# Kernel tuning notes

Hardware: AMD Instinct MI355X
Metric: run time of the kernel (lower is better)

## Reference

```python
import jax, jax.numpy as jnp
import numpy as np

B = 16384       # batch size
P = 2           # fixed pooling factor per bag (offsets are arange * P)
NTAB = 26       # number of sparse feature tables
NROWS = 100000  # rows per embedding table
D = 128         # embedding dim == ln_bot[-1]
LN_BOT = [13, 512, 256, 128]
LN_TOP = [479, 1024, 512, 256, 1]


def setup_inputs() -> dict:
    key = jax.random.key(0)
    ks = jax.random.split(key, 32)
    inp = {}
    inp['dense_x'] = jax.random.normal(ks[0], (B, LN_BOT[0]), dtype=jnp.float32)
    # offsets: uniform stride-P bags (EmbeddingBag offsets)
    inp['lS_o'] = jnp.broadcast_to(jnp.arange(B, dtype=jnp.int64) * P, (NTAB, B))
    inp['lS_i'] = jax.random.randint(ks[1], (NTAB, B * P), 0, NROWS, dtype=jnp.int64)
    # embedding tables, uniform(-sqrt(1/n), sqrt(1/n))
    bound = float(np.sqrt(1.0 / NROWS))
    inp['emb_tables'] = jax.random.uniform(ks[2], (NTAB, NROWS, D), dtype=jnp.float32,
                                           minval=-bound, maxval=bound)
    # bot MLP params (He-style scaled normal)
    ki = 3
    for i in range(len(LN_BOT) - 1):
        n, m = LN_BOT[i], LN_BOT[i + 1]
        inp[f'bw{i}'] = jax.random.normal(ks[ki], (m, n), dtype=jnp.float32) * np.sqrt(2.0 / (m + n)); ki += 1
        inp[f'bb{i}'] = jax.random.normal(ks[ki], (m,), dtype=jnp.float32) * np.sqrt(1.0 / m); ki += 1
    for i in range(len(LN_TOP) - 1):
        n, m = LN_TOP[i], LN_TOP[i + 1]
        inp[f'tw{i}'] = jax.random.normal(ks[ki], (m, n), dtype=jnp.float32) * np.sqrt(2.0 / (m + n)); ki += 1
        inp[f'tb{i}'] = jax.random.normal(ks[ki], (m,), dtype=jnp.float32) * np.sqrt(1.0 / m); ki += 1
    return inp


def _mlp(x, Ws, bs, sigmoid_layer):
    for i, (W, b) in enumerate(zip(Ws, bs)):
        x = x @ W.T + b
        x = jax.nn.sigmoid(x) if i == sigmoid_layer else jax.nn.relu(x)
    return x


def reference(dense_x, lS_o, lS_i, emb_tables,
              bw0, bb0, bw1, bb1, bw2, bb2,
              tw0, tb0, tw1, tb1, tw2, tb2, tw3, tb3):
    # bot MLP (sigmoid_bot = -1 -> all ReLU)
    x = _mlp(dense_x, [bw0, bw1, bw2], [bb0, bb1, bb2], sigmoid_layer=-1)  # [B, D]

    # multi-table EmbeddingBag sum pooling. Offsets (lS_o) are uniform stride-P
    # arange bags, so sum pooling is a gather + reshape + sum over P.
    def pool_one(table, idx):
        return table[idx].reshape(B, P, D).sum(axis=1)  # [B, D]
    ly = jax.vmap(pool_one)(emb_tables, lS_i)  # [NTAB, B, D]

    # dot interaction (arch_interaction_itself=False -> strict lower triangle)
    T = jnp.concatenate([x[:, None, :], jnp.transpose(ly, (1, 0, 2))], axis=1)  # [B, 27, D]
    Z = jnp.einsum('bid,bjd->bij', T, T)  # [B, 27, 27]
    ni = NTAB + 1
    li, lj = jnp.tril_indices(ni, k=-1)
    Zflat = Z[:, li, lj]  # [B, 351]
    R = jnp.concatenate([x, Zflat], axis=1)  # [B, 479]

    # top MLP (sigmoid at last layer, sigmoid_top = 3)
    p = _mlp(R, [tw0, tw1, tw2, tw3], [tb0, tb1, tb2, tb3], sigmoid_layer=3)
    return p  # [B, 1]
```

## Files before the change

kernel.cpp:

```cpp
#include <hip/hip_runtime.h>
#include <hip/hip_bf16.h>
#include <math.h>

#define BATCH 16384
#define NTAB 26
#define DIM 128
#define NROWS 100000

typedef short bf16x8 __attribute__((ext_vector_type(8)));
typedef float f32x4 __attribute__((ext_vector_type(4)));
typedef float f32x16 __attribute__((ext_vector_type(16)));

__device__ __forceinline__ ushort f2b(float f) {
  union { float f; unsigned u; } c; c.f = f;
  unsigned r = (c.u + 0x7fffu + ((c.u >> 16) & 1u)) >> 16;
  return (ushort)r;
}
__device__ __forceinline__ float b2f(ushort u) {
  union { unsigned u; float f; } c; c.u = (unsigned)u << 16;
  return c.f;
}

__device__ __forceinline__ void gload_lds16(const void* g, void* l) {
  __builtin_amdgcn_global_load_lds(
      (const __attribute__((address_space(1))) void*)g,
      (__attribute__((address_space(3))) void*)l, 16, 0, 0);
}

__global__ __launch_bounds__(256) void prep_kernel(
    const float* __restrict__ x, const float* __restrict__ W0,
    const float* __restrict__ b0, ushort* __restrict__ y,
    const float* __restrict__ bw1, const float* __restrict__ bw2,
    const float* __restrict__ tw0, const float* __restrict__ tw1,
    const float* __restrict__ tw2,
    ushort* __restrict__ o1, ushort* __restrict__ o2, ushort* __restrict__ o3,
    ushort* __restrict__ o4, ushort* __restrict__ o5) {
  int blk = blockIdx.x;
  if (blk < 2 * BATCH) {
    int b = blk >> 1;
    int m = ((blk & 1) << 8) | threadIdx.x;
    const float* xr = x + (size_t)b * 13;
    const float* wr = W0 + (size_t)m * 13;
    float acc = b0[m];
#pragma unroll
    for (int k = 0; k < 13; k++) acc = fmaf(xr[k], wr[k], acc);
    y[(size_t)b * 512 + m] = f2b(fmaxf(acc, 0.f));
    return;
  }
  int cb = blk - 2 * BATCH;
  int c = cb >> 11;
  int i = (cb & 2047) * 256 + threadIdx.x;
  switch (c) {
    case 0: if (i < 256 * 512) o1[i] = f2b(bw1[i]); break;
    case 1: if (i < 128 * 256) o2[i] = f2b(bw2[i]); break;
    case 2: if (i < 1024 * 512) {
      int r = i >> 9, cc = i & 511;
      o3[i] = (cc < 479) ? f2b(tw0[(size_t)r * 479 + cc]) : (ushort)0;
    } break;
    case 3: if (i < 512 * 1024) o4[i] = f2b(tw1[i]); break;
    case 4: if (i < 256 * 512) o5[i] = f2b(tw2[i]); break;
  }
}

__global__ __launch_bounds__(256) void embint_kernel(
    const float* __restrict__ tables, const int* __restrict__ lS_i,
    const ushort* __restrict__ xb, ushort* __restrict__ R) {
  __shared__ ushort Tls[4][32 * 128];
  const int wave = threadIdx.x >> 6, lane = threadIdx.x & 63;
  const int b = blockIdx.x * 4 + wave;
  char* tl = (char*)Tls[wave];

  *(uint*)(tl + lane * 4) = *(const uint*)(xb + (size_t)b * 128 + lane * 2);
#pragma unroll
  for (int r = 27; r < 32; r++)
    *(uint*)(tl + r * 256 + ((lane * 4) ^ ((r & 7) << 4))) = 0;
#pragma unroll 8
  for (int t = 0; t < NTAB; t++) {
    const int* idx = lS_i + ((size_t)t << 15) + (b << 1);
    int i0 = idx[0], i1 = idx[1];
    float2 v0 = ((const float2*)(tables + ((size_t)t * NROWS + i0) * DIM))[lane];
    float2 v1 = ((const float2*)(tables + ((size_t)t * NROWS + i1) * DIM))[lane];
    ushort2 s; s.x = f2b(v0.x + v1.x); s.y = f2b(v0.y + v1.y);
    int row = t + 1;
    *(uint*)(tl + row * 256 + ((lane * 4) ^ ((row & 7) << 4))) = *(uint*)&s;
  }
  __syncthreads();

  const int row = lane & 31;
  const int khb = (lane >> 5) * 16;
  const int swz = (row & 7) << 4;
  f32x16 z = {};
#pragma unroll
  for (int ks = 0; ks < 8; ks++) {
    bf16x8 a = *(const bf16x8*)(tl + row * 256 + ((ks * 32 + khb) ^ swz));
    z = __builtin_amdgcn_mfma_f32_32x32x16_bf16(a, a, z, 0, 0, 0);
  }

  ushort* Rb = R + (size_t)b * 512;
  *(uint*)(Rb + lane * 2) = *(const uint*)(tl + lane * 4);
  if (lane < 33) Rb[479 + lane] = 0;
  const int j = lane & 31;
  const int rb4 = (lane >> 5) * 4;
#pragma unroll
  for (int r = 0; r < 16; r++) {
    int i = (r & 3) + 8 * (r >> 2) + rb4;
    if (i <= 26 && j < i) Rb[DIM + (i * (i - 1)) / 2 + j] = f2b(z[r]);
  }
}

#define SLOT_BYTES 49152
template <int ACT>
__global__ __launch_bounds__(512, 2) void gemm256_kernel(
    const ushort* __restrict__ A, const ushort* __restrict__ W,
    const float* __restrict__ bias, ushort* __restrict__ C, int K, int ldc) {
  __shared__ char lds[3 * SLOT_BYTES];
  const int tid = threadIdx.x;
  const int lane = tid & 63, wid = tid >> 6;
  const int wm = wid >> 2, wn = wid & 3;

  const int nwg = gridDim.x * gridDim.y;
  const int orig = blockIdx.y * gridDim.x + blockIdx.x;
  const int q = nwg >> 3, r8 = nwg & 7;
  const int xcd = orig & 7, pos = orig >> 3;
  const int swzid = (xcd < r8 ? xcd * (q + 1) : r8 * (q + 1) + (xcd - r8) * q) + pos;
  const int m0 = (swzid / gridDim.x) * 256, n0 = (swzid % gridDim.x) * 128;
  const int NK = K >> 6;

  const int srow = tid >> 3;
  const int scolb = (tid & 7) << 4;

#pragma unroll
  for (int kt = 0; kt < 2; kt++) {
    char* As = lds + kt * SLOT_BYTES;
    char* Bs = As + 32768;
    const int k0 = kt * 64;
#pragma unroll
    for (int i = 0; i < 4; i++) {
      int row = i * 64 + srow;
      int colb = scolb ^ ((row & 7) << 4);
      gload_lds16(A + (size_t)(m0 + row) * K + k0 + (colb >> 1), As + i * 8192 + wid * 1024);
    }
#pragma unroll
    for (int i = 0; i < 2; i++) {
      int row = i * 64 + srow;
      int colb = scolb ^ ((row & 7) << 4);
      gload_lds16(W + (size_t)(n0 + row) * K + k0 + (colb >> 1), Bs + i * 8192 + wid * 1024);
    }
  }

  f32x4 acc[8][2] = {};
  const int fr = lane & 15;
  const int fkb = (lane >> 4) * 16;

  for (int kt = 0; kt < NK; kt++) {
    if (kt + 1 < NK) { asm volatile("s_waitcnt vmcnt(6)" ::: "memory"); }
    else             { asm volatile("s_waitcnt vmcnt(0)" ::: "memory"); }
    __builtin_amdgcn_sched_barrier(0);
    __builtin_amdgcn_s_barrier();
    __builtin_amdgcn_sched_barrier(0);

    const char* As = lds + (kt % 3) * SLOT_BYTES;
    const char* Bs = As + 32768;
    char* Ad = lds + ((kt + 2) % 3) * SLOT_BYTES;
    char* Bd = Ad + 32768;
    const int k2 = (kt + 2) * 64;
    const bool do_stage = (kt + 2 < NK);

#pragma unroll
    for (int kh = 0; kh < 2; kh++) {
      bf16x8 a[8], b[2];
#pragma unroll
      for (int mf = 0; mf < 8; mf++) {
        int row = wm * 128 + mf * 16 + fr;
        int colb = (kh * 64 + fkb) ^ ((row & 7) << 4);
        a[mf] = *(const bf16x8*)(As + row * 128 + colb);
      }
#pragma unroll
      for (int nf = 0; nf < 2; nf++) {
        int row = wn * 32 + nf * 16 + fr;
        int colb = (kh * 64 + fkb) ^ ((row & 7) << 4);
        b[nf] = *(const bf16x8*)(Bs + row * 128 + colb);
      }
      if (do_stage) {
#pragma unroll
        for (int i = kh * 2; i < kh * 2 + 2; i++) {
          int row = i * 64 + srow;
          int colb = scolb ^ ((row & 7) << 4);
          gload_lds16(A + (size_t)(m0 + row) * K + k2 + (colb >> 1), Ad + i * 8192 + wid * 1024);
        }
        {
          int row = kh * 64 + srow;
          int colb = scolb ^ ((row & 7) << 4);
          gload_lds16(W + (size_t)(n0 + row) * K + k2 + (colb >> 1), Bd + kh * 8192 + wid * 1024);
        }
      }
      __builtin_amdgcn_sched_barrier(0);
      __builtin_amdgcn_s_barrier();
      asm volatile("s_waitcnt lgkmcnt(0)" ::: "memory");
      __builtin_amdgcn_sched_barrier(0);
      __builtin_amdgcn_s_setprio(1);
#pragma unroll
      for (int mf = 0; mf < 8; mf++)
#pragma unroll
        for (int nf = 0; nf < 2; nf++)
          acc[mf][nf] = __builtin_amdgcn_mfma_f32_16x16x32_bf16(a[mf], b[nf], acc[mf][nf], 0, 0, 0);
      __builtin_amdgcn_s_setprio(0);
      if (kh == 0) {
        __builtin_amdgcn_sched_barrier(0);
        __builtin_amdgcn_s_barrier();
        __builtin_amdgcn_sched_barrier(0);
      }
    }
  }

  const int cr = lane & 15, rh = (lane >> 4) * 4;
#pragma unroll
  for (int nf = 0; nf < 2; nf++) {
    int n = n0 + wn * 32 + nf * 16 + cr;
    float bs = bias[n];
#pragma unroll
    for (int mf = 0; mf < 8; mf++) {
      int mb = m0 + wm * 128 + mf * 16 + rh;
#pragma unroll
      for (int r = 0; r < 4; r++) {
        float v = acc[mf][nf][r] + bs;
        if (ACT) v = fmaxf(v, 0.f);
        C[(size_t)(mb + r) * ldc + n] = f2b(v);
      }
    }
  }
}

template <int ACT>
__global__ __launch_bounds__(256) void gemm_bf16_kernel(
    const ushort* __restrict__ A, const ushort* __restrict__ W,
    const float* __restrict__ bias, ushort* __restrict__ C, int K, int ldc) {
  __shared__ ushort As[128 * 32];
  __shared__ ushort Bs[128 * 32];
  const int tid = threadIdx.x;
  const int lane = tid & 63, wave = tid >> 6;
  const int m0 = blockIdx.y * 128, n0 = blockIdx.x * 128;
  const int wr = wave >> 1, wc = wave & 1;

  const int srow = lane >> 2;
  const int scolb = ((lane & 3) << 4) ^ ((srow & 3) << 4);
  const ushort* Ag = A + (size_t)(m0 + wave * 16 + srow) * K + (scolb >> 1);
  const ushort* Wg = W + (size_t)(n0 + wave * 16 + srow) * K + (scolb >> 1);
  ushort* AsW = &As[(wave * 16) * 32];
  ushort* BsW = &Bs[(wave * 16) * 32];

  f32x4 acc[4][4] = {};
  const int fr = lane & 15;
  const int fkb = (lane >> 4) * 16;
  const int fswz = (fr & 3) << 4;

  for (int k0 = 0; k0 < K; k0 += 32) {
    gload_lds16(Ag + k0, AsW);
    gload_lds16(Ag + (size_t)64 * K + k0, AsW + 64 * 32);
    gload_lds16(Wg + k0, BsW);
    gload_lds16(Wg + (size_t)64 * K + k0, BsW + 64 * 32);
    __syncthreads();
    bf16x8 a[4], b[4];
#pragma unroll
    for (int i = 0; i < 4; i++) {
      a[i] = *(const bf16x8*)((const char*)As + (wr * 64 + i * 16 + fr) * 64 + (fkb ^ fswz));
      b[i] = *(const bf16x8*)((const char*)Bs + (wc * 64 + i * 16 + fr) * 64 + (fkb ^ fswz));
    }
#pragma unroll
    for (int i = 0; i < 4; i++)
#pragma unroll
      for (int j = 0; j < 4; j++)
        acc[i][j] = __builtin_amdgcn_mfma_f32_16x16x32_bf16(a[i], b[j], acc[i][j], 0, 0, 0);
    __syncthreads();
  }

  const int col_l = lane & 15, row_h = (lane >> 4) * 4;
#pragma unroll
  for (int j = 0; j < 4; j++) {
    int n = n0 + wc * 64 + j * 16 + col_l;
    float bs = bias[n];
#pragma unroll
    for (int i = 0; i < 4; i++) {
      int mbase = m0 + wr * 64 + i * 16 + row_h;
#pragma unroll
      for (int r = 0; r < 4; r++) {
        float v = acc[i][j][r] + bs;
        if (ACT) v = fmaxf(v, 0.f);
        C[(size_t)(mbase + r) * ldc + n] = f2b(v);
      }
    }
  }
}

__global__ __launch_bounds__(256) void t2final_kernel(
    const ushort* __restrict__ A, const ushort* __restrict__ W,
    const float* __restrict__ bias, const float* __restrict__ w3,
    const float* __restrict__ b3, float* __restrict__ out) {
  __shared__ char smem[64 * 264 * 2];
  ushort* As = (ushort*)smem;
  ushort* Bs = (ushort*)(smem + 4096);
  ushort* Ct = (ushort*)smem;
  const int tid = threadIdx.x;
  const int lane = tid & 63, wave = tid >> 6;
  const int m0 = blockIdx.x * 64;

  const int srow = lane >> 2;
  const int scolb = ((lane & 3) << 4) ^ ((srow & 3) << 4);
  const ushort* Ag = A + (size_t)(m0 + wave * 16 + srow) * 512 + (scolb >> 1);
  const ushort* Wg = W + (size_t)(wave * 16 + srow) * 512 + (scolb >> 1);

  f32x4 acc[4][4] = {};
  const int fr = lane & 15;
  const int fkb = (lane >> 4) * 16;
  const int fswz = (fr & 3) << 4;

  for (int k0 = 0; k0 < 512; k0 += 32) {
    gload_lds16(Ag + k0, (char*)As + wave * 1024);
#pragma unroll
    for (int i = 0; i < 4; i++)
      gload_lds16(Wg + (size_t)(i * 64) * 512 + k0, (char*)Bs + i * 4096 + wave * 1024);
    __syncthreads();
    bf16x8 a[4], b[4];
#pragma unroll
    for (int i = 0; i < 4; i++) {
      a[i] = *(const bf16x8*)((const char*)As + (i * 16 + fr) * 64 + (fkb ^ fswz));
      b[i] = *(const bf16x8*)((const char*)Bs + (wave * 64 + i * 16 + fr) * 64 + (fkb ^ fswz));
    }
#pragma unroll
    for (int i = 0; i < 4; i++)
#pragma unroll
      for (int j = 0; j < 4; j++)
        acc[i][j] = __builtin_amdgcn_mfma_f32_16x16x32_bf16(a[i], b[j], acc[i][j], 0, 0, 0);
    __syncthreads();
  }

  const int col_l = lane & 15, row_h = (lane >> 4) * 4;
#pragma unroll
  for (int j = 0; j < 4; j++) {
    int n = wave * 64 + j * 16 + col_l;
    float bs = bias[n];
#pragma unroll
    for (int i = 0; i < 4; i++) {
      int mb = i * 16 + row_h;
#pragma unroll
      for (int r = 0; r < 4; r++)
        Ct[(size_t)(mb + r) * 264 + n] = f2b(fmaxf(acc[i][j][r] + bs, 0.f));
    }
  }
  __syncthreads();

  const float4 wv = ((const float4*)w3)[lane];
  const float bf = b3[0];
  for (int rr = 0; rr < 16; rr++) {
    int row = wave * 16 + rr;
    ushort4 a4 = *(const ushort4*)&Ct[(size_t)row * 264 + lane * 4];
    float s = b2f(a4.x) * wv.x + b2f(a4.y) * wv.y + b2f(a4.z) * wv.z + b2f(a4.w) * wv.w;
#pragma unroll
    for (int off = 32; off >= 1; off >>= 1) s += __shfl_xor(s, off);
    if (lane == 0) out[m0 + row] = 1.f / (1.f + expf(-(s + bf)));
  }
}

extern "C" void kernel_launch(void* const* d_in, const int* in_sizes, int n_in,
                              void* d_out, int out_size, void* d_ws, size_t ws_size,
                              hipStream_t stream) {
  const float* dense_x = (const float*)d_in[0];
  const int* lS_i = (const int*)d_in[2];
  const float* emb = (const float*)d_in[3];
  const float* bw0 = (const float*)d_in[4];
  const float* bb0 = (const float*)d_in[5];
  const float* bw1 = (const float*)d_in[6];
  const float* bb1 = (const float*)d_in[7];
  const float* bw2 = (const float*)d_in[8];
  const float* bb2 = (const float*)d_in[9];
  const float* tw0 = (const float*)d_in[10];
  const float* tb0 = (const float*)d_in[11];
  const float* tw1 = (const float*)d_in[12];
  const float* tb1 = (const float*)d_in[13];
  const float* tw2 = (const float*)d_in[14];
  const float* tb2 = (const float*)d_in[15];
  const float* tw3 = (const float*)d_in[16];
  const float* tb3 = (const float*)d_in[17];
  float* out = (float*)d_out;

  char* w = (char*)d_ws;
  ushort* xb  = (ushort*)w; w += (size_t)BATCH * 128 * 2;
  ushort* x1  = (ushort*)w; w += (size_t)BATCH * 512 * 2;
  ushort* x2  = (ushort*)w; w += (size_t)BATCH * 256 * 2;
  ushort* R   = (ushort*)w; w += (size_t)BATCH * 512 * 2;
  ushort* t1  = (ushort*)w; w += (size_t)BATCH * 1024 * 2;
  ushort* wb1 = (ushort*)w; w += 256 * 512 * 2;
  ushort* wb2 = (ushort*)w; w += 128 * 256 * 2;
  ushort* wt0 = (ushort*)w; w += 1024 * 512 * 2;
  ushort* wt1 = (ushort*)w; w += 512 * 1024 * 2;
  ushort* wt2 = (ushort*)w; w += 256 * 512 * 2;
  ushort* t2 = x1;

  prep_kernel<<<2 * BATCH + 5 * 2048, 256, 0, stream>>>(
      dense_x, bw0, bb0, x1, bw1, bw2, tw0, tw1, tw2, wb1, wb2, wt0, wt1, wt2);

  gemm_bf16_kernel<1><<<dim3(2, BATCH / 128), 256, 0, stream>>>(x1, wb1, bb1, x2, 512, 256);
  gemm_bf16_kernel<1><<<dim3(1, BATCH / 128), 256, 0, stream>>>(x2, wb2, bb2, xb, 256, 128);

  embint_kernel<<<BATCH / 4, 256, 0, stream>>>(emb, lS_i, xb, R);

  gemm256_kernel<1><<<dim3(1024 / 128, BATCH / 256), 512, 0, stream>>>(R,  wt0, tb0, t1, 512, 1024);
  gemm256_kernel<1><<<dim3(512 / 128,  BATCH / 256), 512, 0, stream>>>(t1, wt1, tb1, t2, 1024, 512);
  t2final_kernel<<<BATCH / 64, 256, 0, stream>>>(t2, wt2, tb2, tw3, tb3, out);
}
```

Baseline: 218.1 us.

## Fuse bottom MLP layers 1 and 2 into one pipelined kernel

Replaces the two separate bottom-MLP GEMM launches with one kernel. Each 64-row block computes the 512→256 layer into LDS and then the 256→128 layer straight from LDS. The first layer uses a triple-buffered async global-to-LDS pipeline, and the second-layer weight is pre-swizzled in the prep kernel so it loads directly into a conflict-free LDS layout. This removes the x2 intermediate round trip through global memory and one launch. In exchange it uses a large LDS footprint (about 160KB) and runs only 256 blocks, which limits occupancy.

```diff
diff --git a/kernel.cpp b/kernel.cpp
--- a/kernel.cpp
+++ b/kernel.cpp
@@ -52,7 +52,11 @@
   int i = (cb & 2047) * 256 + threadIdx.x;
   switch (c) {
     case 0: if (i < 256 * 512) o1[i] = f2b(bw1[i]); break;
-    case 1: if (i < 128 * 256) o2[i] = f2b(bw2[i]); break;
+    case 1: if (i < 128 * 256) {
+      int r = i >> 8, cc = i & 255;
+      int db = (((cc << 1) ^ ((r & 7) << 4)) >> 1);
+      o2[r * 256 + db] = f2b(bw2[i]);
+    } break;
     case 2: if (i < 1024 * 512) {
       int r = i >> 9, cc = i & 511;
       o3[i] = (cc < 479) ? f2b(tw0[(size_t)r * 479 + cc]) : (ushort)0;
@@ -105,6 +109,130 @@
   for (int r = 0; r < 16; r++) {
     int i = (r & 3) + 8 * (r >> 2) + rb4;
     if (i <= 26 && j < i) Rb[DIM + (i * (i - 1)) / 2 + j] = f2b(z[r]);
+  }
+}
+
+#define BMLP_SLOT 20480
+__global__ __launch_bounds__(256) void bmlp_kernel(
+    const ushort* __restrict__ A, const ushort* __restrict__ W1,
+    const float* __restrict__ b1, const ushort* __restrict__ W2g,
+    const float* __restrict__ b2, ushort* __restrict__ Y) {
+  __shared__ char lds[3 * BMLP_SLOT + 64 * 260 * 2 + 65536];
+  char* C1 = lds + 3 * BMLP_SLOT;
+  char* W2s = C1 + 64 * 260 * 2;
+  const int tid = threadIdx.x;
+  const int lane = tid & 63, wave = tid >> 6;
+  const int m0 = blockIdx.x * 64;
+
+  const int srow = lane >> 2;
+  const int scolb = ((lane & 3) << 4) ^ ((srow & 3) << 4);
+
+#pragma unroll
+  for (int i = 0; i < 16; i++)
+    gload_lds16(W2g + i * 2048 + wave * 512 + lane * 8, W2s + i * 4096 + wave * 1024);
+
+#pragma unroll
+  for (int kt = 0; kt < 2; kt++) {
+    char* As = lds + kt * BMLP_SLOT;
+    char* W1s = As + 4096;
+    const int k0 = kt * 32;
+    gload_lds16(A + (size_t)(m0 + wave * 16 + srow) * 512 + k0 + (scolb >> 1),
+                As + wave * 1024);
+#pragma unroll
+    for (int i = 0; i < 4; i++)
+      gload_lds16(W1 + (size_t)(wave * 64 + i * 16 + srow) * 512 + k0 + (scolb >> 1),
+                  W1s + wave * 4096 + i * 1024);
+  }
+
+  f32x4 acc1[4][4] = {};
+  const int fr = lane & 15;
+  const int fkb = (lane >> 4) * 16;
+  const int fswz = (fr & 3) << 4;
+
+  for (int kt = 0; kt < 16; kt++) {
+    if (kt < 15) { asm volatile("s_waitcnt vmcnt(5)" ::: "memory"); }
+    else         { asm volatile("s_waitcnt vmcnt(0)" ::: "memory"); }
+    __builtin_amdgcn_sched_barrier(0);
+    __builtin_amdgcn_s_barrier();
+    __builtin_amdgcn_sched_barrier(0);
+
+    const char* As = lds + (kt % 3) * BMLP_SLOT;
+    const char* W1s = As + 4096;
+    bf16x8 a[4], w[4];
+#pragma unroll
+    for (int i = 0; i < 4; i++)
+      a[i] = *(const bf16x8*)(As + (i * 16 + fr) * 64 + (fkb ^ fswz));
+#pragma unroll
+    for (int j = 0; j < 4; j++)
+      w[j] = *(const bf16x8*)(W1s + (wave * 64 + j * 16 + fr) * 64 + (fkb ^ fswz));
+
+    if (kt + 2 < 16) {
+      char* Ad = lds + ((kt + 2) % 3) * BMLP_SLOT;
+      char* W1d = Ad + 4096;
+      const int k2 = (kt + 2) * 32;
+      gload_lds16(A + (size_t)(m0 + wave * 16 + srow) * 512 + k2 + (scolb >> 1),
+                  Ad + wave * 1024);
+#pragma unroll
+      for (int i = 0; i < 4; i++)
+        gload_lds16(W1 + (size_t)(wave * 64 + i * 16 + srow) * 512 + k2 + (scolb >> 1),
+                    W1d + wave * 4096 + i * 1024);
+    }
+
+    asm volatile("s_waitcnt lgkmcnt(0)" ::: "memory");
+    __builtin_amdgcn_sched_barrier(0);
+    __builtin_amdgcn_s_setprio(1);
+#pragma unroll
+    for (int i = 0; i < 4; i++)
+#pragma unroll
+      for (int j = 0; j < 4; j++)
+        acc1[i][j] = __builtin_amdgcn_mfma_f32_16x16x32_bf16(a[i], w[j], acc1[i][j], 0, 0, 0);
+    __builtin_amdgcn_s_setprio(0);
+  }
+
+  const int col_l = lane & 15, row_h = (lane >> 4) * 4;
+#pragma unroll
+  for (int j = 0; j < 4; j++) {
+    int n = wave * 64 + j * 16 + col_l;
+    float bs = b1[n];
+#pragma unroll
+    for (int i = 0; i < 4; i++) {
+      int rw = i * 16 + row_h;
+#pragma unroll
+      for (int r = 0; r < 4; r++)
+        *(ushort*)(C1 + (size_t)(rw + r) * 520 + n * 2) = f2b(fmaxf(acc1[i][j][r] + bs, 0.f));
+    }
+  }
+  __syncthreads();
+
+  f32x4 acc2[4][2] = {};
+#pragma unroll
+  for (int ks = 0; ks < 8; ks++) {
+    const int kb = ks * 64 + fkb;
+    bf16x8 a2[4], w2[2];
+#pragma unroll
+    for (int i = 0; i < 4; i++)
+      a2[i] = *(const bf16x8*)(C1 + (i * 16 + fr) * 520 + kb);
+#pragma unroll
+    for (int j = 0; j < 2; j++)
+      w2[j] = *(const bf16x8*)(W2s + (wave * 32 + j * 16 + fr) * 512 + (kb ^ ((fr & 7) << 4)));
+#pragma unroll
+    for (int i = 0; i < 4; i++)
+#pragma unroll
+      for (int j = 0; j < 2; j++)
+        acc2[i][j] = __builtin_amdgcn_mfma_f32_16x16x32_bf16(a2[i], w2[j], acc2[i][j], 0, 0, 0);
+  }
+
+#pragma unroll
+  for (int j = 0; j < 2; j++) {
+    int n = wave * 32 + j * 16 + col_l;
+    float bs = b2[n];
+#pragma unroll
+    for (int i = 0; i < 4; i++) {
+      int mb = m0 + i * 16 + row_h;
+#pragma unroll
+      for (int r = 0; r < 4; r++)
+        Y[(size_t)(mb + r) * 128 + n] = f2b(fmaxf(acc2[i][j][r] + bs, 0.f));
+    }
   }
 }
 
@@ -226,67 +354,6 @@
         float v = acc[mf][nf][r] + bs;
         if (ACT) v = fmaxf(v, 0.f);
         C[(size_t)(mb + r) * ldc + n] = f2b(v);
-      }
-    }
-  }
-}
-
-template <int ACT>
-__global__ __launch_bounds__(256) void gemm_bf16_kernel(
-    const ushort* __restrict__ A, const ushort* __restrict__ W,
-    const float* __restrict__ bias, ushort* __restrict__ C, int K, int ldc) {
-  __shared__ ushort As[128 * 32];
-  __shared__ ushort Bs[128 * 32];
-  const int tid = threadIdx.x;
-  const int lane = tid & 63, wave = tid >> 6;
-  const int m0 = blockIdx.y * 128, n0 = blockIdx.x * 128;
-  const int wr = wave >> 1, wc = wave & 1;
-
-  const int srow = lane >> 2;
-  const int scolb = ((lane & 3) << 4) ^ ((srow & 3) << 4);
-  const ushort* Ag = A + (size_t)(m0 + wave * 16 + srow) * K + (scolb >> 1);
-  const ushort* Wg = W + (size_t)(n0 + wave * 16 + srow) * K + (scolb >> 1);
-  ushort* AsW = &As[(wave * 16) * 32];
-  ushort* BsW = &Bs[(wave * 16) * 32];
-
-  f32x4 acc[4][4] = {};
-  const int fr = lane & 15;
-  const int fkb = (lane >> 4) * 16;
-  const int fswz = (fr & 3) << 4;
-
-  for (int k0 = 0; k0 < K; k0 += 32) {
-    gload_lds16(Ag + k0, AsW);
-    gload_lds16(Ag + (size_t)64 * K + k0, AsW + 64 * 32);
-    gload_lds16(Wg + k0, BsW);
-    gload_lds16(Wg + (size_t)64 * K + k0, BsW + 64 * 32);
-    __syncthreads();
-    bf16x8 a[4], b[4];
-#pragma unroll
-    for (int i = 0; i < 4; i++) {
-      a[i] = *(const bf16x8*)((const char*)As + (wr * 64 + i * 16 + fr) * 64 + (fkb ^ fswz));
-      b[i] = *(const bf16x8*)((const char*)Bs + (wc * 64 + i * 16 + fr) * 64 + (fkb ^ fswz));
-    }
-#pragma unroll
-    for (int i = 0; i < 4; i++)
-#pragma unroll
-      for (int j = 0; j < 4; j++)
-        acc[i][j] = __builtin_amdgcn_mfma_f32_16x16x32_bf16(a[i], b[j], acc[i][j], 0, 0, 0);
-    __syncthreads();
-  }
-
-  const int col_l = lane & 15, row_h = (lane >> 4) * 4;
-#pragma unroll
-  for (int j = 0; j < 4; j++) {
-    int n = n0 + wc * 64 + j * 16 + col_l;
-    float bs = bias[n];
-#pragma unroll
-    for (int i = 0; i < 4; i++) {
-      int mbase = m0 + wr * 64 + i * 16 + row_h;
-#pragma unroll
-      for (int r = 0; r < 4; r++) {
-        float v = acc[i][j][r] + bs;
-        if (ACT) v = fmaxf(v, 0.f);
-        C[(size_t)(mbase + r) * ldc + n] = f2b(v);
       }
     }
   }
@@ -395,12 +462,12 @@
   ushort* wt1 = (ushort*)w; w += 512 * 1024 * 2;
   ushort* wt2 = (ushort*)w; w += 256 * 512 * 2;
   ushort* t2 = x1;
+  (void)x2;
 
   prep_kernel<<<2 * BATCH + 5 * 2048, 256, 0, stream>>>(
       dense_x, bw0, bb0, x1, bw1, bw2, tw0, tw1, tw2, wb1, wb2, wt0, wt1, wt2);
 
-  gemm_bf16_kernel<1><<<dim3(2, BATCH / 128), 256, 0, stream>>>(x1, wb1, bb1, x2, 512, 256);
-  gemm_bf16_kernel<1><<<dim3(1, BATCH / 128), 256, 0, stream>>>(x2, wb2, bb2, xb, 256, 128);
+  bmlp_kernel<<<BATCH / 64, 256, 0, stream>>>(x1, wb1, bb1, wb2, bb2, xb);
 
   embint_kernel<<<BATCH / 4, 256, 0, stream>>>(emb, lS_i, xb, R);
 
```

Result: faster. 204.8 us (-6.1%).
